# Kernel tuning notes

Hardware: AMD Instinct MI355X
Metric: run time of the kernel (lower is better)

## Reference

```python
import jax, jax.numpy as jnp
import numpy as np

RAY_START, RAY_END = 2.25, 3.3
DEPTH_RES, N_IMPORTANCE = 48, 48
BOX_WARP = 1.0
PLANE_AXES = jnp.array([[[1.,0.,0.],[0.,1.,0.],[0.,0.,1.]],
                        [[1.,0.,0.],[0.,0.,1.],[0.,1.,0.]],
                        [[0.,0.,1.],[1.,0.,0.],[0.,1.,0.]]], jnp.float32)


def grid_sample_bilinear(feat, gx, gy):
    # feat [B,C,H,W]; gx,gy [B,M] in [-1,1]; bilinear, zeros padding, align_corners=False
    B, C, H, W = feat.shape
    x = (gx + 1.0) * (W * 0.5) - 0.5
    y = (gy + 1.0) * (H * 0.5) - 0.5
    x0 = jnp.floor(x); y0 = jnp.floor(y)
    wx = (x - x0)[:, None, :]; wy = (y - y0)[:, None, :]
    x0i = x0.astype(jnp.int32); y0i = y0.astype(jnp.int32)
    flat = feat.reshape(B, C, H * W)
    def gather(xi, yi):
        valid = ((xi >= 0) & (xi < W) & (yi >= 0) & (yi < H)).astype(feat.dtype)
        idx = jnp.clip(yi, 0, H - 1) * W + jnp.clip(xi, 0, W - 1)
        v = jnp.take_along_axis(flat, jnp.broadcast_to(idx[:, None, :], (B, C, idx.shape[-1])), axis=2)
        return v * valid[:, None, :]
    v00 = gather(x0i, y0i); v10 = gather(x0i + 1, y0i)
    v01 = gather(x0i, y0i + 1); v11 = gather(x0i + 1, y0i + 1)
    return (v00 * (1 - wx) * (1 - wy) + v10 * wx * (1 - wy)
            + v01 * (1 - wx) * wy + v11 * wx * wy)  # [B,C,M]


def sample_from_planes(planes_feat, coords):
    # planes_feat [N,3,C,H,W], coords [N,M,3] -> [N,3,M,C]
    N, P, C, H, W = planes_feat.shape
    M = coords.shape[1]
    c = (2.0 / BOX_WARP) * coords
    inv = jnp.linalg.inv(PLANE_AXES)  # [P,3,3]
    proj = jnp.einsum('nmi,pij->npmj', c, inv)[..., :2]
    out = grid_sample_bilinear(planes_feat.reshape(N * P, C, H, W),
                               proj[..., 0].reshape(N * P, M),
                               proj[..., 1].reshape(N * P, M))
    return out.reshape(N, P, C, M).transpose(0, 1, 3, 2)


def decode(feats, w1, b1, w2, b2):
    # OSGDecoder: mean over planes, Linear->softplus->Linear
    x = feats.mean(axis=1)
    h = jax.nn.softplus(x @ w1 + b1)
    o = h @ w2 + b2
    sigma = o[..., :1]
    rgb = jax.nn.sigmoid(o[..., 1:]) * (1 + 2 * 0.001) - 0.001
    return rgb, sigma


def ray_march(colors, densities, depths, color_bg=None):
    # MipRayMarcher2 with softplus density clamp and BG compositing via final transmittance
    deltas = depths[:, :, 1:] - depths[:, :, :-1]
    colors_mid = 0.5 * (colors[:, :, :-1] + colors[:, :, 1:])
    densities_mid = jax.nn.softplus(0.5 * (densities[:, :, :-1] + densities[:, :, 1:]) - 1.0)
    depths_mid = 0.5 * (depths[:, :, :-1] + depths[:, :, 1:])
    alpha = 1.0 - jnp.exp(-densities_mid * deltas)
    alpha_shifted = jnp.concatenate([jnp.ones_like(alpha[:, :, :1]), 1 - alpha + 1e-10], axis=2)
    T = jnp.cumprod(alpha_shifted, axis=2)
    weights = alpha * T[:, :, :-1]
    comp_rgb = (weights * colors_mid).sum(axis=2)
    weight_total = weights.sum(axis=2)
    comp_depth = jnp.nan_to_num((weights * depths_mid).sum(axis=2) / weight_total, nan=float('inf'))
    comp_depth = jnp.clip(comp_depth, depths.min(), depths.max())
    bg_trans = T[:, :, -1]  # [B,R,1]
    if color_bg is not None:
        comp_rgb = comp_rgb + bg_trans * color_bg
    comp_rgb = comp_rgb * 2.0 - 1.0
    return comp_rgb, comp_depth, weights, alpha, bg_trans


def sample_pdf(bins, weights, n_importance, eps=1e-5):
    # inverse-CDF importance sampling (deterministic midpoint u)
    nw = weights.shape[-1]
    weights = weights + eps
    pdf = weights / weights.sum(axis=-1, keepdims=True)
    cdf = jnp.concatenate([jnp.zeros_like(pdf[:, :1]), jnp.cumsum(pdf, axis=-1)], axis=-1)
    u = (jnp.arange(n_importance, dtype=cdf.dtype) + 0.5) / n_importance
    u = jnp.broadcast_to(u, (cdf.shape[0], n_importance))
    inds = jax.vmap(lambda c, uu: jnp.searchsorted(c, uu, side='right'))(cdf, u)
    below = jnp.clip(inds - 1, 0, nw)
    above = jnp.clip(inds, 0, nw)
    cdf_b = jnp.take_along_axis(cdf, below, axis=-1)
    cdf_a = jnp.take_along_axis(cdf, above, axis=-1)
    bins_b = jnp.take_along_axis(bins, below, axis=-1)
    bins_a = jnp.take_along_axis(bins, above, axis=-1)
    denom = jnp.where(cdf_a - cdf_b < eps, 1.0, cdf_a - cdf_b)
    return bins_b + (u - cdf_b) / denom * (bins_a - bins_b)


def sample_importance(z_vals, weights, n_importance):
    B, R, S, _ = z_vals.shape
    z = z_vals.reshape(B * R, S)
    w = weights.reshape(B * R, -1) + 0.01
    wp = jnp.pad(w, ((0, 0), (1, 1)), constant_values=-np.inf)
    w = jnp.maximum(wp[:, :-1], wp[:, 1:])      # max_pool1d(k=2,s=1,p=1)
    w = 0.5 * (w[:, :-1] + w[:, 1:]) + 0.01     # avg_pool1d(k=2,s=1)
    z_mid = 0.5 * (z[:, :-1] + z[:, 1:])
    z_fine = sample_pdf(z_mid, w[:, 1:-1], n_importance)
    return jax.lax.stop_gradient(z_fine).reshape(B, R, n_importance, 1)


def unify_samples(d1, c1, s1, d2, c2, s2):
    depths = jnp.concatenate([d1, d2], axis=2)
    colors = jnp.concatenate([c1, c2], axis=2)
    dens = jnp.concatenate([s1, s2], axis=2)
    idx = jnp.argsort(depths, axis=2)
    depths = jnp.take_along_axis(depths, idx, axis=2)
    colors = jnp.take_along_axis(colors, jnp.broadcast_to(idx, colors.shape), axis=2)
    dens = jnp.take_along_axis(dens, idx, axis=2)
    return depths, colors, dens


def sample_stratified(B, R, dtype):
    S = DEPTH_RES
    delta = (RAY_END - RAY_START) / (S - 1)
    d = jnp.linspace(RAY_START, RAY_END, S, dtype=dtype).reshape(1, 1, S, 1) + 0.5 * delta
    return jnp.broadcast_to(d, (B, R, S, 1))


def setup_inputs() -> dict:
    key = jax.random.key(0)
    ks = jax.random.split(key, 10)
    B, R, C, H = 4, 4096, 32, 256
    planes = 0.1 * jax.random.normal(ks[0], (B, 3, C, H, H), jnp.float32)
    ray_origins = jnp.array([0.0, 0.0, 2.7]) + 0.03 * jax.random.normal(ks[1], (B, R, 3), jnp.float32)
    uv = jax.random.uniform(ks[2], (B, R, 2), jnp.float32, -0.4, 0.4)
    d = jnp.concatenate([uv, -jnp.ones((B, R, 1), jnp.float32)], axis=-1)
    ray_directions = d / jnp.linalg.norm(d, axis=-1, keepdims=True)
    z_bg = jax.random.normal(ks[3], (B, 64), jnp.float32)
    dec_w1 = jax.random.normal(ks[4], (C, 64), jnp.float32) / np.sqrt(C)
    dec_b1 = jnp.zeros((64,), jnp.float32)
    dec_w2 = jax.random.normal(ks[5], (64, 33), jnp.float32) / 8.0
    dec_b2 = jnp.zeros((33,), jnp.float32)
    bg_w1 = jax.random.normal(ks[6], (67, 64), jnp.float32) / np.sqrt(67)
    bg_b1 = jnp.zeros((64,), jnp.float32)
    bg_w2 = jax.random.normal(ks[7], (64, 32), jnp.float32) / 8.0
    bg_b2 = jnp.zeros((32,), jnp.float32)
    return dict(planes=planes, ray_origins=ray_origins, ray_directions=ray_directions, z_bg=z_bg,
                dec_w1=dec_w1, dec_b1=dec_b1, dec_w2=dec_w2, dec_b2=dec_b2,
                bg_w1=bg_w1, bg_b1=bg_b1, bg_w2=bg_w2, bg_b2=bg_b2)


def reference(planes, ray_origins, ray_directions, z_bg, dec_w1, dec_b1, dec_w2, dec_b2,
              bg_w1, bg_b1, bg_w2, bg_b2):
    B, R, _ = ray_origins.shape
    S = DEPTH_RES
    depths_coarse = sample_stratified(B, R, planes.dtype)
    coords = (ray_origins[:, :, None, :] + depths_coarse * ray_directions[:, :, None, :]).reshape(B, -1, 3)
    feats = sample_from_planes(planes, coords)
    rgb_c, sig_c = decode(feats, dec_w1, dec_b1, dec_w2, dec_b2)
    rgb_c = rgb_c.reshape(B, R, S, -1)
    sig_c = sig_c.reshape(B, R, S, 1)
    # Ball background feature: MLP on [dir, z_bg]
    z = jnp.broadcast_to(z_bg[:, None, :], (B, R, z_bg.shape[-1]))
    hb = jax.nn.softplus(jnp.concatenate([ray_directions, z], axis=-1) @ bg_w1 + bg_b1)
    color_bg = jax.nn.sigmoid(hb @ bg_w2 + bg_b2)  # [B,R,32]
    _, _, w_coarse, _, _ = ray_march(rgb_c, sig_c, depths_coarse)
    depths_fine = sample_importance(depths_coarse, w_coarse, N_IMPORTANCE)
    coords_f = (ray_origins[:, :, None, :] + depths_fine * ray_directions[:, :, None, :]).reshape(B, -1, 3)
    feats_f = sample_from_planes(planes, coords_f)
    rgb_f, sig_f = decode(feats_f, dec_w1, dec_b1, dec_w2, dec_b2)
    rgb_f = rgb_f.reshape(B, R, N_IMPORTANCE, -1)
    sig_f = sig_f.reshape(B, R, N_IMPORTANCE, 1)
    depths_all, rgb_all, sig_all = unify_samples(depths_coarse, rgb_c, sig_c, depths_fine, rgb_f, sig_f)
    rgb_final, depth_final, weights, alpha, bg_T = ray_march(rgb_all, sig_all, depths_all, color_bg)
    return rgb_final, depth_final, weights.sum(axis=2)
```

## Files before the change

kernel.cpp:

```cpp
#include <hip/hip_runtime.h>
#include <hip/hip_bf16.h>
#include <math.h>

#define NB 4
#define NR 4096
#define NC 32
#define NH 256
#define NW 256
#define NS 48
#define NRAYS (NB*NR)
#define NSAMP (NRAYS*NS)

__device__ __forceinline__ float coarse_depth(int i) {
    const float DELTA = 1.05f / 47.f;
    return 2.25f + i * DELTA + 0.5f * DELTA;
}
__device__ __forceinline__ float zmid_c(int i) {
    return 0.5f * (coarse_depth(i) + coarse_depth(i + 1));
}
__device__ __forceinline__ float softplus_f(float x) {
    return fmaxf(x, 0.f) + __logf(1.f + __expf(-fabsf(x)));
}
__device__ __forceinline__ float sigmoid_f(float x) {
    return __frcp_rn(1.f + __expf(-x));
}

__global__ __launch_bounds__(256) void k_transpose(const float* __restrict__ in,
                                                   float* __restrict__ out) {
    __shared__ float tile[32][65];
    int bp = blockIdx.x >> 10;
    int t0 = (blockIdx.x & 1023) * 64;
    const float* src = in + (size_t)bp * NC * NH * NW;
    float* dst = out + (size_t)bp * NH * NW * NC;
    int px = threadIdx.x & 63;
    int c0 = threadIdx.x >> 6;
    #pragma unroll
    for (int cc = 0; cc < 32; cc += 4)
        tile[cc + c0][px] = src[(size_t)(cc + c0) * NH * NW + t0 + px];
    __syncthreads();
    int c = threadIdx.x & 31;
    int p0 = threadIdx.x >> 5;
    #pragma unroll
    for (int pp = 0; pp < 64; pp += 8)
        dst[(size_t)(t0 + pp + p0) * NC + c] = tile[c][pp + p0];
}

__device__ __forceinline__ float tapv(const float* __restrict__ base,
                                      int xi, int yi, int c) {
    bool valid = (xi >= 0) & (xi < NW) & (yi >= 0) & (yi < NH);
    int xc = min(max(xi, 0), NW - 1);
    int yc = min(max(yi, 0), NH - 1);
    float v = base[((size_t)yc * NW + xc) * NC + c];
    return valid ? v : 0.f;
}

template<bool FINE>
__global__ __launch_bounds__(256) void k_sample_decode(
    const float* __restrict__ planes_t,
    const float* __restrict__ origins,
    const float* __restrict__ dirs,
    const float* __restrict__ dfine,
    const float* __restrict__ w1, const float* __restrict__ b1,
    const float* __restrict__ w2, const float* __restrict__ b2,
    float* __restrict__ rgb_out, float* __restrict__ sig_out)
{
    __shared__ float xbuf[256][33];
    __shared__ float w1s[2048];
    __shared__ float w2s[2112];
    __shared__ float b1s[64];
    __shared__ float b2s[33];
    for (int i = threadIdx.x; i < 2048; i += 256) w1s[i] = w1[i];
    for (int i = threadIdx.x; i < 2112; i += 256) w2s[i] = w2[i];
    if (threadIdx.x < 64) b1s[threadIdx.x] = b1[threadIdx.x];
    if (threadIdx.x < 33) b2s[threadIdx.x] = b2[threadIdx.x];
    __syncthreads();

    int lane = threadIdx.x & 31;
    int hw = threadIdx.x >> 5;

    #pragma unroll 1
    for (int it = 0; it < 32; ++it) {
        int ls = it * 8 + hw;
        int s = blockIdx.x * 256 + ls;
        int ray = s / NS;
        int k = s - ray * NS;
        float t = FINE ? dfine[s] : coarse_depth(k);
        float ox = origins[ray*3+0], oy = origins[ray*3+1], oz = origins[ray*3+2];
        float ddx = dirs[ray*3+0],   ddy = dirs[ray*3+1],   ddz = dirs[ray*3+2];
        float cx = 2.f * (ox + t * ddx);
        float cy = 2.f * (oy + t * ddy);
        float cz = 2.f * (oz + t * ddz);
        int bi = ray >> 12;
        float acc = 0.f;
        #pragma unroll
        for (int p = 0; p < 3; ++p) {
            float gx = (p == 2) ? cz : cx;
            float gy = (p == 0) ? cy : ((p == 1) ? cz : cx);
            float fx = (gx + 1.f) * 128.f - 0.5f;
            float fy = (gy + 1.f) * 128.f - 0.5f;
            float x0f = floorf(fx), y0f = floorf(fy);
            float wx = fx - x0f, wy = fy - y0f;
            int x0 = (int)x0f, y0 = (int)y0f;
            if (x0 >= -1 && x0 <= NW - 1 && y0 >= -1 && y0 <= NH - 1) {
                const float* base = planes_t + (size_t)(bi * 3 + p) * NH * NW * NC;
                float v00 = tapv(base, x0,     y0,     lane);
                float v10 = tapv(base, x0 + 1, y0,     lane);
                float v01 = tapv(base, x0,     y0 + 1, lane);
                float v11 = tapv(base, x0 + 1, y0 + 1, lane);
                acc += v00*(1.f-wx)*(1.f-wy) + v10*wx*(1.f-wy)
                     + v01*(1.f-wx)*wy       + v11*wx*wy;
            }
        }
        xbuf[ls][lane] = acc / 3.f;
    }
    __syncthreads();

    float x[32];
    #pragma unroll
    for (int c = 0; c < 32; ++c) x[c] = xbuf[threadIdx.x][c];
    float o[33];
    #pragma unroll
    for (int k2 = 0; k2 < 33; ++k2) o[k2] = b2s[k2];
    #pragma unroll 1
    for (int j = 0; j < 64; ++j) {
        float a = b1s[j];
        #pragma unroll
        for (int c = 0; c < 32; ++c) a += x[c] * w1s[c * 64 + j];
        float h = softplus_f(a);
        #pragma unroll
        for (int k2 = 0; k2 < 33; ++k2) o[k2] += h * w2s[j * 33 + k2];
    }
    int sg = blockIdx.x * 256 + threadIdx.x;
    sig_out[sg] = o[0];
    #pragma unroll
    for (int c = 0; c < 32; ++c)
        xbuf[threadIdx.x][c] = sigmoid_f(o[1 + c]) * 1.002f - 0.001f;
    __syncthreads();
    #pragma unroll 1
    for (int it = 0; it < 32; ++it) {
        int ls = it * 8 + hw;
        rgb_out[(size_t)(blockIdx.x * 256 + ls) * 32 + lane] = xbuf[ls][lane];
    }
}

__global__ __launch_bounds__(256) void k_importance(const float* __restrict__ sig,
                                                    float* __restrict__ dfine) {
    int ray = blockIdx.x * 256 + threadIdx.x;
    const float* sp = sig + (size_t)ray * NS;
    float w[47];
    float T = 1.f;
    float sprev = sp[0];
    #pragma unroll
    for (int i = 0; i < 47; ++i) {
        float scur = sp[i + 1];
        float dens = softplus_f(0.5f * (sprev + scur) - 1.f);
        float delta = coarse_depth(i + 1) - coarse_depth(i);
        float alpha = 1.f - __expf(-dens * delta);
        w[i] = alpha * T + 0.01f;
        T *= (1.f - alpha + 1e-10f);
        sprev = scur;
    }
    float p[45];
    float sum = 0.f;
    #pragma unroll
    for (int i = 1; i <= 45; ++i) {
        float nwi  = fmaxf(w[i - 1], w[i]);
        float nwi1 = fmaxf(w[i], w[i + 1]);
        float wb = 0.5f * (nwi + nwi1) + 0.01f;
        float v = wb + 1e-5f;
        p[i - 1] = v;
        sum += v;
    }
    int k = 0;
    float cdf_lo = 0.f;
    #pragma unroll
    for (int i = 0; i < 45; ++i) {
        float cdf_hi = cdf_lo + p[i] / sum;
        float bb = zmid_c(i), ba = zmid_c(i + 1);
        float denom = cdf_hi - cdf_lo;
        if (denom < 1e-5f) denom = 1.f;
        while (k < 48) {
            float u = (k + 0.5f) / 48.f;
            if (u < cdf_hi) {
                dfine[(size_t)ray * NS + k] = bb + (u - cdf_lo) / denom * (ba - bb);
                ++k;
            } else break;
        }
        cdf_lo = cdf_hi;
    }
    while (k < 48) {
        dfine[(size_t)ray * NS + k] = zmid_c(45);
        ++k;
    }
}

__global__ __launch_bounds__(256) void k_final(
    const float* __restrict__ sig_c, const float* __restrict__ rgb_c,
    const float* __restrict__ sig_f, const float* __restrict__ rgb_f,
    const float* __restrict__ dfine,
    const float* __restrict__ dirs, const float* __restrict__ z_bg,
    const float* __restrict__ bw1, const float* __restrict__ bb1,
    const float* __restrict__ bw2, const float* __restrict__ bb2,
    float* __restrict__ out_rgb, float* __restrict__ out_dep,
    float* __restrict__ out_wt)
{
    __shared__ float s_d[4][96];
    __shared__ float s_sig[4][96];
    __shared__ int   s_src[4][96];
    __shared__ float s_fine[4][48];
    __shared__ float s_w[4][96];
    __shared__ float s_g[4][96];
    __shared__ float s_h[4][64];
    __shared__ float s_zb[64];
    int lane = threadIdx.x & 63;
    int wv = threadIdx.x >> 6;
    int ray = blockIdx.x * 4 + wv;
    int bi = (blockIdx.x * 4) >> 12;
    if (threadIdx.x < 64) s_zb[threadIdx.x] = z_bg[bi * 64 + threadIdx.x];
    if (lane < 48) s_fine[wv][lane] = dfine[(size_t)ray * NS + lane];
    __syncthreads();

    if (lane < 48) {
        float cd = coarse_depth(lane);
        int lo = 0, hi = 48;
        while (lo < hi) { int mid = (lo + hi) >> 1;
            if (s_fine[wv][mid] < cd) lo = mid + 1; else hi = mid; }
        int rc = lane + lo;
        s_d[wv][rc] = cd;
        s_sig[wv][rc] = sig_c[(size_t)ray * NS + lane];
        s_src[wv][rc] = lane;
        float f = s_fine[wv][lane];
        lo = 0; hi = 48;
        while (lo < hi) { int mid = (lo + hi) >> 1;
            if (coarse_depth(mid) <= f) lo = mid + 1; else hi = mid; }
        int rf = lane + lo;
        s_d[wv][rf] = f;
        s_sig[wv][rf] = sig_f[(size_t)ray * NS + lane];
        s_src[wv][rf] = 48 + lane;
    }
    float ddx = dirs[ray*3+0], ddy = dirs[ray*3+1], ddz = dirs[ray*3+2];
    __syncthreads();

    float alpha0 = 0.f, alpha1 = 0.f, a0 = 1.f, a1 = 1.f;
    float dm0 = 0.f, dm1 = 0.f;
    if (lane < 48) {
        int i0 = 2 * lane, i1 = i0 + 1;
        float d0 = s_d[wv][i0], sA = s_sig[wv][i0];
        float d1 = s_d[wv][i1], sB = s_sig[wv][i1];
        {
            float dens = softplus_f(0.5f * (sA + sB) - 1.f);
            alpha0 = 1.f - __expf(-dens * (d1 - d0));
            a0 = 1.f - alpha0 + 1e-10f;
            dm0 = 0.5f * (d0 + d1);
        }
        if (i1 < 95) {
            float d2 = s_d[wv][i1 + 1], sC = s_sig[wv][i1 + 1];
            float dens = softplus_f(0.5f * (sB + sC) - 1.f);
            alpha1 = 1.f - __expf(-dens * (d2 - d1));
            a1 = 1.f - alpha1 + 1e-10f;
            dm1 = 0.5f * (d1 + d2);
        }
    }
    float P = a0 * a1;
    #pragma unroll
    for (int off = 1; off < 64; off <<= 1) {
        float t = __shfl_up(P, off);
        if (lane >= off) P *= t;
    }
    float T_all = __shfl(P, 63);
    float E = __shfl_up(P, 1);
    if (lane == 0) E = 1.f;
    float w0 = alpha0 * E;
    float w1 = alpha1 * (E * a0);
    float sw = w0 + w1;
    float sd = w0 * dm0 + w1 * dm1;
    #pragma unroll
    for (int off = 32; off; off >>= 1) {
        sw += __shfl_xor(sw, off);
        sd += __shfl_xor(sd, off);
    }
    if (lane < 48) {
        s_w[wv][2 * lane] = w0;
        s_w[wv][2 * lane + 1] = w1;
    }
    __syncthreads();
    {
        int i = lane;
        float wm = (i > 0) ? s_w[wv][i - 1] : 0.f;
        s_g[wv][i] = 0.5f * (wm + s_w[wv][i]);
        int i2 = lane + 64;
        if (lane < 32)
            s_g[wv][i2] = 0.5f * (s_w[wv][i2 - 1] + s_w[wv][i2]);
    }

    float a = bb1[lane] + ddx * bw1[lane] + ddy * bw1[64 + lane] + ddz * bw1[128 + lane];
    #pragma unroll 1
    for (int i = 0; i < 64; ++i) a += s_zb[i] * bw1[(3 + i) * 64 + lane];
    s_h[wv][lane] = softplus_f(a);
    __syncthreads();
    int c = lane & 31;
    float ob = bb2[c];
    #pragma unroll 1
    for (int j = 0; j < 64; ++j) ob += s_h[wv][j] * bw2[j * 32 + c];
    float bgc = sigmoid_f(ob);

    int h = lane >> 5;
    size_t rbase = (size_t)ray * NS * 32;
    const float* b0p = rgb_c + rbase;
    const float* b1p = rgb_f + rbase - (size_t)48 * 32;
    float acc = 0.f;
    #pragma unroll 4
    for (int i = h; i < 96; i += 2) {
        int src = s_src[wv][i];
        const float* cp = ((src < 48) ? b0p : b1p) + (size_t)src * 32;
        acc += s_g[wv][i] * cp[c];
    }
    acc += __shfl_xor(acc, 32);

    float rgbv = (acc + T_all * bgc) * 2.f - 1.f;
    float dep = sd / sw;
    if (!(dep == dep)) dep = INFINITY;
    dep = fminf(fmaxf(dep, coarse_depth(0)), coarse_depth(47));
    if (lane < 32) out_rgb[(size_t)ray * 32 + c] = rgbv;
    if (lane == 0) { out_dep[ray] = dep; out_wt[ray] = sw; }
}

extern "C" void kernel_launch(void* const* d_in, const int* in_sizes, int n_in,
                              void* d_out, int out_size, void* d_ws, size_t ws_size,
                              hipStream_t stream) {
    (void)in_sizes; (void)n_in; (void)out_size; (void)ws_size;
    const float* planes  = (const float*)d_in[0];
    const float* origins = (const float*)d_in[1];
    const float* dirs    = (const float*)d_in[2];
    const float* z_bg    = (const float*)d_in[3];
    const float* dw1     = (const float*)d_in[4];
    const float* db1     = (const float*)d_in[5];
    const float* dw2     = (const float*)d_in[6];
    const float* db2     = (const float*)d_in[7];
    const float* bw1     = (const float*)d_in[8];
    const float* bb1     = (const float*)d_in[9];
    const float* bw2     = (const float*)d_in[10];
    const float* bb2     = (const float*)d_in[11];

    char* ws = (char*)d_ws;
    size_t off = 0;
    float* planes_t = (float*)(ws + off); off += (size_t)NB * 3 * NH * NW * NC * 4;
    float* rgb_c    = (float*)(ws + off); off += (size_t)NSAMP * 32 * 4;
    float* rgb_f    = (float*)(ws + off); off += (size_t)NSAMP * 32 * 4;
    float* sig_c    = (float*)(ws + off); off += (size_t)NSAMP * 4;
    float* sig_f    = (float*)(ws + off); off += (size_t)NSAMP * 4;
    float* dfine    = (float*)(ws + off); off += (size_t)NSAMP * 4;

    float* out_rgb = (float*)d_out;
    float* out_dep = out_rgb + (size_t)NRAYS * 32;
    float* out_wt  = out_dep + NRAYS;

    k_transpose<<<dim3(NB * 3 * 1024), dim3(256), 0, stream>>>(planes, planes_t);
    k_sample_decode<false><<<dim3(NSAMP / 256), dim3(256), 0, stream>>>(
        planes_t, origins, dirs, (const float*)nullptr,
        dw1, db1, dw2, db2, rgb_c, sig_c);
    k_importance<<<dim3(NRAYS / 256), dim3(256), 0, stream>>>(sig_c, dfine);
    k_sample_decode<true><<<dim3(NSAMP / 256), dim3(256), 0, stream>>>(
        planes_t, origins, dirs, dfine,
        dw1, db1, dw2, db2, rgb_f, sig_f);
    k_final<<<dim3(NRAYS / 4), dim3(256), 0, stream>>>(
        sig_c, rgb_c, sig_f, rgb_f, dfine, dirs, z_bg,
        bw1, bb1, bw2, bb2, out_rgb, out_dep, out_wt);
}
```

Before: 905.7 us.

## Precompute per-sample bilinear taps, shuffle-broadcast them, and skip the MLP for empty samples

Each thread now computes coordinates, bilinear weights and base offsets for its own sample once. The 64-lane wave then broadcasts these with shuffles, so each wave gathers two samples per step instead of every half-wave recomputing the projection. Samples that fall outside all three planes skip the decoder MLP and use a constant output precomputed by a small new kernel from the biases. Decoder weights are stored transposed and padded in shared memory for contiguous reads. The cost is extra shuffles and divergence between empty and non-empty samples within a wave.

```diff
diff --git a/kernel.cpp b/kernel.cpp
--- a/kernel.cpp
+++ b/kernel.cpp
@@ -45,13 +45,20 @@
         dst[(size_t)(t0 + pp + p0) * NC + c] = tile[c][pp + p0];
 }
 
-__device__ __forceinline__ float tapv(const float* __restrict__ base,
-                                      int xi, int yi, int c) {
-    bool valid = (xi >= 0) & (xi < NW) & (yi >= 0) & (yi < NH);
-    int xc = min(max(xi, 0), NW - 1);
-    int yc = min(max(yi, 0), NH - 1);
-    float v = base[((size_t)yc * NW + xc) * NC + c];
-    return valid ? v : 0.f;
+__global__ __launch_bounds__(64) void k_const(const float* __restrict__ b1,
+                                              const float* __restrict__ w2,
+                                              const float* __restrict__ b2,
+                                              float* __restrict__ const_o) {
+    __shared__ float h[64];
+    int j = threadIdx.x;
+    h[j] = softplus_f(b1[j]);
+    __syncthreads();
+    if (j < 33) {
+        float o = b2[j];
+        #pragma unroll 1
+        for (int i = 0; i < 64; ++i) o += h[i] * w2[i * 33 + j];
+        const_o[j] = (j == 0) ? o : sigmoid_f(o) * 1.002f - 0.001f;
+    }
 }
 
 template<bool FINE>
@@ -62,84 +69,127 @@
     const float* __restrict__ dfine,
     const float* __restrict__ w1, const float* __restrict__ b1,
     const float* __restrict__ w2, const float* __restrict__ b2,
+    const float* __restrict__ const_o,
     float* __restrict__ rgb_out, float* __restrict__ sig_out)
 {
     __shared__ float xbuf[256][33];
-    __shared__ float w1s[2048];
-    __shared__ float w2s[2112];
+    __shared__ float w1t[64][32];
+    __shared__ float w2p[64][36];
     __shared__ float b1s[64];
-    __shared__ float b2s[33];
-    for (int i = threadIdx.x; i < 2048; i += 256) w1s[i] = w1[i];
-    for (int i = threadIdx.x; i < 2112; i += 256) w2s[i] = w2[i];
+    __shared__ float b2s[36];
+    __shared__ float cbuf[36];
+
+    for (int i = threadIdx.x; i < 2048; i += 256) {
+        int j = i >> 5, c = i & 31;
+        w1t[j][c] = w1[c * 64 + j];
+    }
+    for (int i = threadIdx.x; i < 64 * 36; i += 256) {
+        int j = i / 36, kx = i - j * 36;
+        w2p[j][kx] = (kx < 33) ? w2[j * 33 + kx] : 0.f;
+    }
     if (threadIdx.x < 64) b1s[threadIdx.x] = b1[threadIdx.x];
-    if (threadIdx.x < 33) b2s[threadIdx.x] = b2[threadIdx.x];
-    __syncthreads();
-
-    int lane = threadIdx.x & 31;
-    int hw = threadIdx.x >> 5;
-
+    if (threadIdx.x < 36) {
+        b2s[threadIdx.x]  = (threadIdx.x < 33) ? b2[threadIdx.x] : 0.f;
+        cbuf[threadIdx.x] = (threadIdx.x < 33) ? const_o[threadIdx.x] : 0.f;
+    }
+
+    int lane  = threadIdx.x & 63;
+    int wbase = threadIdx.x & 192;
+    int s0    = blockIdx.x * 256 + wbase;
+
+    int s   = s0 + lane;
+    int ray = s / NS;
+    int kk  = s - ray * NS;
+    float t = FINE ? dfine[s] : coarse_depth(kk);
+    float ox = origins[ray*3+0], oy = origins[ray*3+1], oz = origins[ray*3+2];
+    float ddx = dirs[ray*3+0],   ddy = dirs[ray*3+1],   ddz = dirs[ray*3+2];
+    float cx = 2.f * (ox + t * ddx);
+    float cy = 2.f * (oy + t * ddy);
+    float cz = 2.f * (oz + t * ddz);
+    int bi = ray >> 12;
+    int   m_base[3];
+    float m_q[3][4];
+    #pragma unroll
+    for (int p = 0; p < 3; ++p) {
+        float gx = (p == 2) ? cz : cx;
+        float gy = (p == 0) ? cy : ((p == 1) ? cz : cx);
+        float fx = (gx + 1.f) * 128.f - 0.5f;
+        float fy = (gy + 1.f) * 128.f - 0.5f;
+        float x0f = floorf(fx), y0f = floorf(fy);
+        float wx = fx - x0f, wy = fy - y0f;
+        int x0 = (int)x0f, y0 = (int)y0f;
+        if (x0 >= -1 && x0 <= 255 && y0 >= -1 && y0 <= 255) {
+            float wxm = 1.f - wx, wym = 1.f - wy;
+            float q00 = wxm*wym, q10 = wx*wym, q01 = wxm*wy, q11 = wx*wy;
+            if (!(x0 >= 0   && y0 >= 0))   q00 = 0.f;
+            if (!(x0 <= 254 && y0 >= 0))   q10 = 0.f;
+            if (!(x0 >= 0   && y0 <= 254)) q01 = 0.f;
+            if (!(x0 <= 254 && y0 <= 254)) q11 = 0.f;
+            m_base[p] = (bi*3 + p) * (NH*NW*NC) + (y0*NW + x0)*NC;
+            m_q[p][0] = q00; m_q[p][1] = q10; m_q[p][2] = q01; m_q[p][3] = q11;
+        } else {
+            m_base[p] = -1;
+            m_q[p][0] = m_q[p][1] = m_q[p][2] = m_q[p][3] = 0.f;
+        }
+    }
+
+    int ch   = lane & 31;
+    int half = lane >> 5;
     #pragma unroll 1
-    for (int it = 0; it < 32; ++it) {
-        int ls = it * 8 + hw;
-        int s = blockIdx.x * 256 + ls;
-        int ray = s / NS;
-        int k = s - ray * NS;
-        float t = FINE ? dfine[s] : coarse_depth(k);
-        float ox = origins[ray*3+0], oy = origins[ray*3+1], oz = origins[ray*3+2];
-        float ddx = dirs[ray*3+0],   ddy = dirs[ray*3+1],   ddz = dirs[ray*3+2];
-        float cx = 2.f * (ox + t * ddx);
-        float cy = 2.f * (oy + t * ddy);
-        float cz = 2.f * (oz + t * ddz);
-        int bi = ray >> 12;
+    for (int i = 0; i < 64; i += 2) {
+        int src = i + half;
         float acc = 0.f;
         #pragma unroll
         for (int p = 0; p < 3; ++p) {
-            float gx = (p == 2) ? cz : cx;
-            float gy = (p == 0) ? cy : ((p == 1) ? cz : cx);
-            float fx = (gx + 1.f) * 128.f - 0.5f;
-            float fy = (gy + 1.f) * 128.f - 0.5f;
-            float x0f = floorf(fx), y0f = floorf(fy);
-            float wx = fx - x0f, wy = fy - y0f;
-            int x0 = (int)x0f, y0 = (int)y0f;
-            if (x0 >= -1 && x0 <= NW - 1 && y0 >= -1 && y0 <= NH - 1) {
-                const float* base = planes_t + (size_t)(bi * 3 + p) * NH * NW * NC;
-                float v00 = tapv(base, x0,     y0,     lane);
-                float v10 = tapv(base, x0 + 1, y0,     lane);
-                float v01 = tapv(base, x0,     y0 + 1, lane);
-                float v11 = tapv(base, x0 + 1, y0 + 1, lane);
-                acc += v00*(1.f-wx)*(1.f-wy) + v10*wx*(1.f-wy)
-                     + v01*(1.f-wx)*wy       + v11*wx*wy;
+            int   bse = __shfl(m_base[p], src);
+            float q00 = __shfl(m_q[p][0], src);
+            float q10 = __shfl(m_q[p][1], src);
+            float q01 = __shfl(m_q[p][2], src);
+            float q11 = __shfl(m_q[p][3], src);
+            if (bse >= 0) {
+                const float* ptr = planes_t + (size_t)bse + ch;
+                acc += q00 * ptr[0]    + q10 * ptr[32]
+                     + q01 * ptr[8192] + q11 * ptr[8224];
             }
         }
-        xbuf[ls][lane] = acc / 3.f;
-    }
-    __syncthreads();
-
-    float x[32];
-    #pragma unroll
-    for (int c = 0; c < 32; ++c) x[c] = xbuf[threadIdx.x][c];
-    float o[33];
-    #pragma unroll
-    for (int k2 = 0; k2 < 33; ++k2) o[k2] = b2s[k2];
+        xbuf[wbase + i + half][ch] = acc * (1.f / 3.f);
+    }
+    __syncthreads();
+
+    bool empty = (m_base[0] < 0) & (m_base[1] < 0) & (m_base[2] < 0);
+    float sig;
+    if (!empty) {
+        float x[32];
+        #pragma unroll
+        for (int c = 0; c < 32; ++c) x[c] = xbuf[threadIdx.x][c];
+        float o[36];
+        #pragma unroll
+        for (int k2 = 0; k2 < 36; ++k2) o[k2] = b2s[k2];
+        #pragma unroll 1
+        for (int j = 0; j < 64; ++j) {
+            float a = b1s[j];
+            #pragma unroll
+            for (int c = 0; c < 32; ++c) a += x[c] * w1t[j][c];
+            float h = softplus_f(a);
+            #pragma unroll
+            for (int k2 = 0; k2 < 36; ++k2) o[k2] += h * w2p[j][k2];
+        }
+        sig = o[0];
+        #pragma unroll
+        for (int c = 0; c < 32; ++c)
+            xbuf[threadIdx.x][c] = sigmoid_f(o[1 + c]) * 1.002f - 0.001f;
+    } else {
+        sig = cbuf[0];
+        #pragma unroll
+        for (int c = 0; c < 32; ++c) xbuf[threadIdx.x][c] = cbuf[1 + c];
+    }
+    sig_out[s] = sig;
+    __syncthreads();
+
     #pragma unroll 1
-    for (int j = 0; j < 64; ++j) {
-        float a = b1s[j];
-        #pragma unroll
-        for (int c = 0; c < 32; ++c) a += x[c] * w1s[c * 64 + j];
-        float h = softplus_f(a);
-        #pragma unroll
-        for (int k2 = 0; k2 < 33; ++k2) o[k2] += h * w2s[j * 33 + k2];
-    }
-    int sg = blockIdx.x * 256 + threadIdx.x;
-    sig_out[sg] = o[0];
-    #pragma unroll
-    for (int c = 0; c < 32; ++c)
-        xbuf[threadIdx.x][c] = sigmoid_f(o[1 + c]) * 1.002f - 0.001f;
-    __syncthreads();
-    #pragma unroll 1
-    for (int it = 0; it < 32; ++it) {
-        int ls = it * 8 + hw;
-        rgb_out[(size_t)(blockIdx.x * 256 + ls) * 32 + lane] = xbuf[ls][lane];
+    for (int i = 0; i < 64; i += 2) {
+        int r = wbase + i + half;
+        rgb_out[(size_t)(blockIdx.x * 256 + r) * 32 + ch] = xbuf[r][ch];
     }
 }
 
@@ -344,25 +394,27 @@
 
     char* ws = (char*)d_ws;
     size_t off = 0;
+    float* sig_c    = (float*)(ws + off); off += (size_t)NSAMP * 4;
+    float* sig_f    = (float*)(ws + off); off += (size_t)NSAMP * 4;
+    float* dfine    = (float*)(ws + off); off += (size_t)NSAMP * 4;
+    float* const_o  = (float*)(ws + off); off += 4096;
     float* planes_t = (float*)(ws + off); off += (size_t)NB * 3 * NH * NW * NC * 4;
     float* rgb_c    = (float*)(ws + off); off += (size_t)NSAMP * 32 * 4;
     float* rgb_f    = (float*)(ws + off); off += (size_t)NSAMP * 32 * 4;
-    float* sig_c    = (float*)(ws + off); off += (size_t)NSAMP * 4;
-    float* sig_f    = (float*)(ws + off); off += (size_t)NSAMP * 4;
-    float* dfine    = (float*)(ws + off); off += (size_t)NSAMP * 4;
 
     float* out_rgb = (float*)d_out;
     float* out_dep = out_rgb + (size_t)NRAYS * 32;
     float* out_wt  = out_dep + NRAYS;
 
+    k_const<<<dim3(1), dim3(64), 0, stream>>>(db1, dw2, db2, const_o);
     k_transpose<<<dim3(NB * 3 * 1024), dim3(256), 0, stream>>>(planes, planes_t);
     k_sample_decode<false><<<dim3(NSAMP / 256), dim3(256), 0, stream>>>(
         planes_t, origins, dirs, (const float*)nullptr,
-        dw1, db1, dw2, db2, rgb_c, sig_c);
+        dw1, db1, dw2, db2, const_o, rgb_c, sig_c);
     k_importance<<<dim3(NRAYS / 256), dim3(256), 0, stream>>>(sig_c, dfine);
     k_sample_decode<true><<<dim3(NSAMP / 256), dim3(256), 0, stream>>>(
         planes_t, origins, dirs, dfine,
-        dw1, db1, dw2, db2, rgb_f, sig_f);
+        dw1, db1, dw2, db2, const_o, rgb_f, sig_f);
     k_final<<<dim3(NRAYS / 4), dim3(256), 0, stream>>>(
         sig_c, rgb_c, sig_f, rgb_f, dfine, dirs, z_bg,
         bw1, bb1, bw2, bb2, out_rgb, out_dep, out_wt);
```

Result: no change. 893.7 us (-1.3%).
